# Kernel tuning notes

Hardware: AMD Instinct MI355X
Metric: run time of the kernel (lower is better)

The kernel has to match this reference:

```python
import jax, jax.numpy as jnp
import numpy as np
import math

L = 6          # num_layers
D = 512        # hidden_dim
S = 2048       # seq_len
B = 8          # batch
ODIM = 1       # output_dim
SCALES = (24.0, 720.0)


def setup_inputs() -> dict:
    key = jax.random.key(0)
    ks = jax.random.split(key, 12)
    def n(k, shape, scale=0.02):
        return jax.random.normal(k, shape, dtype=jnp.float32) * scale
    return {
        "z": jax.random.normal(ks[0], (B, S, 1), dtype=jnp.float32),
        "c": jax.random.normal(ks[1], (B, S, 1), dtype=jnp.float32),
        "enc_w": n(ks[2], (D, 2)), "enc_b": jnp.zeros((D,), jnp.float32),
        "beta": jnp.ones((L, len(SCALES)), jnp.float32),
        "wq": n(ks[3], (L, D, D)), "bq": jnp.zeros((L, D), jnp.float32),
        "wk": n(ks[4], (L, D, D)), "bk": jnp.zeros((L, D), jnp.float32),
        "wv": n(ks[5], (L, D, D)), "bv": jnp.zeros((L, D), jnp.float32),
        "ln1_w": jnp.ones((L, D), jnp.float32), "ln1_b": jnp.zeros((L, D), jnp.float32),
        "ln2_w": jnp.ones((L, D), jnp.float32), "ln2_b": jnp.zeros((L, D), jnp.float32),
        "ff1_w": n(ks[6], (L, 4 * D, D)), "ff1_b": jnp.zeros((L, 4 * D), jnp.float32),
        "ff2_w": n(ks[7], (L, D, 4 * D)), "ff2_b": jnp.zeros((L, D), jnp.float32),
        "out_w": n(ks[8], (ODIM, D)), "out_b": jnp.zeros((ODIM,), jnp.float32),
    }


def _ln(x, w, b, eps=1e-5):
    m = jnp.mean(x, axis=-1, keepdims=True)
    v = jnp.var(x, axis=-1, keepdims=True)
    return (x - m) * jax.lax.rsqrt(v + eps) * w + b


def _posenc(seq_len, dim):
    pos = jnp.arange(seq_len, dtype=jnp.float32)[:, None]
    div = jnp.exp(jnp.arange(0, dim, 2, dtype=jnp.float32) * (-(math.log(10000.0) / dim)))
    pe = jnp.zeros((seq_len, dim), jnp.float32)
    pe = pe.at[:, 0::2].set(jnp.sin(pos * div))
    pe = pe.at[:, 1::2].set(jnp.cos(pos * div))
    return pe


def reference(z, c, enc_w, enc_b, beta, wq, bq, wk, bk, wv, bv,
              ln1_w, ln1_b, ln2_w, ln2_b, ff1_w, ff1_b, ff2_w, ff2_b,
              out_w, out_b):
    # SequenceEncoder: cat(z,c) -> Linear(2, D) -> + sinusoidal PE
    x = jnp.concatenate([z, c], axis=-1) @ enc_w.T + enc_b       # [B,S,D]
    seq_len, d = x.shape[1], x.shape[2]
    x = x + _posenc(seq_len, d)[None]
    sqrt_d = math.sqrt(d)

    idx = jnp.arange(seq_len, dtype=jnp.float32)
    dist = jnp.abs(idx[:, None] - idx[None, :])                  # [S,S]

    for l in range(L):
        # pre-norm with ln1 (applied twice in the original code - replicated)
        xn = _ln(x, ln1_w[l], ln1_b[l])
        Q = xn @ wq[l].T + bq[l]
        K = xn @ wk[l].T + bk[l]
        V = xn @ wv[l].T + bv[l]
        attn = jnp.einsum('bid,bjd->bij', Q, K) / sqrt_d          # [B,S,S]
        bias = beta[l, 0] * jnp.cos(2.0 * math.pi * dist / SCALES[0]) \
             + beta[l, 1] * jnp.cos(2.0 * math.pi * dist / SCALES[1])
        probs = jax.nn.softmax(attn + bias, axis=-1)
        att_out = jnp.einsum('bij,bjd->bid', probs, V)
        # original applies layer_norm_1 again to the residual sum
        x = _ln(x + att_out, ln1_w[l], ln1_b[l])
        xn2 = _ln(x, ln2_w[l], ln2_b[l])
        h = jax.nn.relu(xn2 @ ff1_w[l].T + ff1_b[l])
        x = x + h @ ff2_w[l].T + ff2_b[l]

    return x @ out_w.T + out_b                                    # [B,S,ODIM]
```

## Files before the change

kernel.cpp:

```cpp
#include <hip/hip_runtime.h>
#include <math.h>

#define BB 8
#define SS 2048
#define DD 512
#define LL 6
#define FFD 2048

typedef _Float16 half_t;
typedef __attribute__((ext_vector_type(8))) _Float16 half8;
typedef __attribute__((ext_vector_type(4))) _Float16 half4;
typedef __attribute__((ext_vector_type(4))) float f32x4;

enum { EPI_NONE = 0, EPI_RELU = 2, EPI_RES = 3, EPI_ATTN = 4, EPI_QKV = 5, EPI_PV = 6 };

__device__ __forceinline__ void gl_lds16(const void* g, void* l) {
    __builtin_amdgcn_global_load_lds(
        (const __attribute__((address_space(1))) unsigned int*)g,
        (__attribute__((address_space(3))) unsigned int*)l,
        16, 0, 0);
}

__device__ __forceinline__ void blockReduce2(float& a, float& b, float* sm) {
#pragma unroll
    for (int off = 32; off; off >>= 1) {
        a += __shfl_down(a, off);
        b += __shfl_down(b, off);
    }
    int lane = threadIdx.x & 63;
    int w = threadIdx.x >> 6;
    if (lane == 0) { sm[w] = a; sm[4 + w] = b; }
    __syncthreads();
    a = sm[0] + sm[1] + sm[2] + sm[3];
    b = sm[4] + sm[5] + sm[6] + sm[7];
    __syncthreads();
}

__global__ __launch_bounds__(256) void encode_kernel(
    const float* __restrict__ z, const float* __restrict__ c,
    const float* __restrict__ enc_w, const float* __restrict__ enc_b,
    float* __restrict__ x)
{
    int idx = blockIdx.x * 256 + threadIdx.x;
    int d  = idx & (DD - 1);
    int bs = idx >> 9;
    int s  = bs & (SS - 1);
    float v = z[bs] * enc_w[2 * d] + c[bs] * enc_w[2 * d + 1] + enc_b[d];
    float div = expf(-(float)(d & ~1) * (9.210340371976184f / 512.0f));
    float ang = (float)s * div;
    v += (d & 1) ? cosf(ang) : sinf(ang);
    x[idx] = v;
}

__global__ __launch_bounds__(256) void convert_layer_kernel(
    const float* __restrict__ wq, const float* __restrict__ wk,
    const float* __restrict__ wv, const float* __restrict__ f1,
    const float* __restrict__ f2, half_t* __restrict__ wqkv,
    half_t* __restrict__ f1h, half_t* __restrict__ f2h)
{
    const int NQ = DD * DD;
    int i = blockIdx.x * 256 + threadIdx.x;
    if (i < 3 * NQ) {
        int which = i >> 18, j = i & (NQ - 1);
        const float* s = (which == 0) ? wq : (which == 1) ? wk : wv;
        wqkv[i] = (half_t)s[j];
    } else {
        int k = i - 3 * NQ;
        if (k < FFD * DD) f1h[k] = (half_t)f1[k];
        else              f2h[k - FFD * DD] = (half_t)f2[k - FFD * DD];
    }
}

__global__ __launch_bounds__(256) void bias_table_kernel(
    const float* __restrict__ beta, float* __restrict__ tbl)
{
    int i = blockIdx.x * 256 + threadIdx.x;
    int l = i >> 11, d = i & (SS - 1);
    tbl[i] = beta[2 * l] * cosf(0.2617993877991494f * d)
           + beta[2 * l + 1] * cosf(0.008726646259971648f * d);
}

__global__ __launch_bounds__(256) void ln_kernel(
    const float* __restrict__ src, const float* __restrict__ w,
    const float* __restrict__ b, half_t* __restrict__ dst)
{
    __shared__ float sm[8];
    size_t row = blockIdx.x;
    const float* p = src + row * DD;
    int t = threadIdx.x;
    float v0 = p[t], v1 = p[t + 256];
    float s = v0 + v1, sq = v0 * v0 + v1 * v1;
    blockReduce2(s, sq, sm);
    float mean = s * (1.0f / DD);
    float var  = sq * (1.0f / DD) - mean * mean;
    float rs   = rsqrtf(var + 1e-5f);
    dst[row * DD + t]       = (half_t)((v0 - mean) * rs * w[t] + b[t]);
    dst[row * DD + t + 256] = (half_t)((v1 - mean) * rs * w[t + 256] + b[t + 256]);
}

__global__ __launch_bounds__(256) void add_ln_ln_kernel(
    float* __restrict__ x, const half_t* __restrict__ att,
    const float* __restrict__ w1, const float* __restrict__ b1,
    const float* __restrict__ w2, const float* __restrict__ b2,
    half_t* __restrict__ xn)
{
    __shared__ float sm[8];
    size_t row = blockIdx.x;
    int t = threadIdx.x;
    float v0 = x[row * DD + t] + (float)att[row * DD + t];
    float v1 = x[row * DD + t + 256] + (float)att[row * DD + t + 256];
    float s = v0 + v1, sq = v0 * v0 + v1 * v1;
    blockReduce2(s, sq, sm);
    float mean = s * (1.0f / DD);
    float var  = sq * (1.0f / DD) - mean * mean;
    float rs   = rsqrtf(var + 1e-5f);
    float y0 = (v0 - mean) * rs * w1[t] + b1[t];
    float y1 = (v1 - mean) * rs * w1[t + 256] + b1[t + 256];
    x[row * DD + t]       = y0;
    x[row * DD + t + 256] = y1;
    s = y0 + y1; sq = y0 * y0 + y1 * y1;
    blockReduce2(s, sq, sm);
    mean = s * (1.0f / DD);
    var  = sq * (1.0f / DD) - mean * mean;
    rs   = rsqrtf(var + 1e-5f);
    xn[row * DD + t]       = (half_t)((y0 - mean) * rs * w2[t] + b2[t]);
    xn[row * DD + t + 256] = (half_t)((y1 - mean) * rs * w2[t + 256] + b2[t + 256]);
}

template<int MT, int EPI, bool OHALF, int SWZ = 0>
__global__ __launch_bounds__(256) void gemm_mfma(
    const half_t* __restrict__ A, const half_t* __restrict__ W,
    const float* __restrict__ bias, const float* __restrict__ res,
    void* __restrict__ Cp, int N, int K, float alpha,
    long long sA, long long sW, long long sC,
    const float* __restrict__ biasK, const float* __restrict__ biasV,
    half_t* __restrict__ Ck, half_t* __restrict__ Cv)
{
    constexpr int TM = MT / 32;
    constexpr int ABUF = MT * 32;
    constexpr int BBUF = 128 * 32;
    __shared__ __align__(16) half_t As[2 * ABUF];
    __shared__ __align__(16) half_t Bs[2 * BBUF];

    int bxi, byi, bzi;
    if (SWZ == 1) {
        const int id = blockIdx.x;
        const int cc = id & 7, rr = id >> 3;
        bxi = rr & 15;
        const int ss = cc + 8 * (rr >> 4);
        byi = ss & 15; bzi = ss >> 4;
    } else { bxi = blockIdx.x; byi = blockIdx.y; bzi = blockIdx.z; }

    const int z = bzi;
    A += (size_t)z * sA; W += (size_t)z * sW;
    float*  Cf = (float*)Cp  + (size_t)z * sC;
    half_t* Ch = (half_t*)Cp + (size_t)z * sC;

    const int tid = threadIdx.x;
    const int wv = tid >> 6, ln = tid & 63;
    const int bm = bxi * MT, bn = byi * 128;
    const int wm = (wv & 1) * (MT / 2), wn = (wv >> 1) * 64;

    const int srow = wv * 16 + (ln >> 2);
    const int scol = (ln & 3) * 8;
    const half_t* Ag = A + (size_t)(bm + srow) * K + scol;
    const half_t* Bg = W + (size_t)(bn + srow) * K + scol;

    f32x4 acc[TM][4] = {};
    float rs[TM];
#pragma unroll
    for (int i = 0; i < TM; ++i) rs[i] = 0.f;

    const int lane15 = ln & 15, quad = ln >> 4;
    const int koff = quad * 8;
    const int nIter = K >> 5;

    {
        char* a = (char*)As + wv * 1024;
        char* b = (char*)Bs + wv * 1024;
        gl_lds16(Ag, a);
        if (MT == 128) gl_lds16(Ag + (size_t)64 * K, a + 4096);
        gl_lds16(Bg, b);
        gl_lds16(Bg + (size_t)64 * K, b + 4096);
    }
    __syncthreads();

    for (int it = 0; it < nIter; ++it) {
        const int cur = it & 1;
        if (it + 1 < nIter) {
            const int k1 = (it + 1) << 5;
            char* a = (char*)As + (cur ^ 1) * (ABUF * 2) + wv * 1024;
            char* b = (char*)Bs + (cur ^ 1) * (BBUF * 2) + wv * 1024;
            gl_lds16(Ag + k1, a);
            if (MT == 128) gl_lds16(Ag + (size_t)64 * K + k1, a + 4096);
            gl_lds16(Bg + k1, b);
            gl_lds16(Bg + (size_t)64 * K + k1, b + 4096);
        }

        const half_t* Ab = As + cur * ABUF;
        const half_t* Bb = Bs + cur * BBUF;
        half8 aF[TM], bF[4];
#pragma unroll
        for (int i = 0; i < TM; ++i)
            aF[i] = *(const half8*)&Ab[(wm + i * 16 + lane15) * 32 + koff];
#pragma unroll
        for (int j = 0; j < 4; ++j)
            bF[j] = *(const half8*)&Bb[(wn + j * 16 + lane15) * 32 + koff];

        if (EPI == EPI_PV) {
#pragma unroll
            for (int i = 0; i < TM; ++i)
#pragma unroll
                for (int e = 0; e < 8; ++e) rs[i] += (float)aF[i][e];
        }

#pragma unroll
        for (int i = 0; i < TM; ++i)
#pragma unroll
            for (int j = 0; j < 4; ++j)
                acc[i][j] = __builtin_amdgcn_mfma_f32_16x16x32_f16(
                    aF[i], bF[j], acc[i][j], 0, 0, 0);

        __syncthreads();
    }

    float inv[TM][4];
    if (EPI == EPI_PV) {
#pragma unroll
        for (int i = 0; i < TM; ++i) {
            rs[i] += __shfl_xor(rs[i], 16);
            rs[i] += __shfl_xor(rs[i], 32);
            rs[i] = 1.0f / rs[i];
#pragma unroll
            for (int r = 0; r < 4; ++r)
                inv[i][r] = __shfl(rs[i], quad * 4 + r);
        }
    }

#pragma unroll
    for (int i = 0; i < TM; ++i) {
        const int m0 = bm + wm + i * 16 + quad * 4;
#pragma unroll
        for (int j = 0; j < 4; ++j) {
            const int gn = bn + wn + j * 16 + lane15;
            if (EPI == EPI_QKV) {
                const int seg = gn >> 9, nn = gn & (DD - 1);
                if (seg == 2) {
                    half4 pk;
#pragma unroll
                    for (int r = 0; r < 4; ++r)
                        pk[r] = (half_t)(acc[i][j][r] + biasV[nn]);
                    const int b = m0 >> 11, s0 = m0 & (SS - 1);
                    *(half4*)&Cv[((size_t)b * DD + nn) * SS + s0] = pk;
                } else {
                    const float bs = (seg == 0) ? bias[nn] : biasK[nn];
                    half_t* dst = (seg == 0) ? Ch : Ck;
#pragma unroll
                    for (int r = 0; r < 4; ++r)
                        dst[(size_t)(m0 + r) * DD + nn] = (half_t)(acc[i][j][r] + bs);
                }
            } else {
#pragma unroll
                for (int r = 0; r < 4; ++r) {
                    const int gm = m0 + r;
                    float v = acc[i][j][r];
                    if (EPI == EPI_ATTN) {
                        int dist = gm - gn; if (dist < 0) dist = -dist;
                        v = __expf(fminf(v * alpha + bias[dist], 10.0f));
                    } else if (EPI == EPI_PV) {
                        v *= inv[i][r];
                    } else {
                        if (EPI == EPI_RELU) v = fmaxf(v + bias[gn], 0.0f);
                        if (EPI == EPI_RES)  v += bias[gn] + res[(size_t)gm * N + gn];
                    }
                    if (OHALF) Ch[(size_t)gm * N + gn] = (half_t)v;
                    else       Cf[(size_t)gm * N + gn] = v;
                }
            }
        }
    }
}

__global__ __launch_bounds__(256) void out_kernel(
    const float* __restrict__ x, const float* __restrict__ ow,
    const float* __restrict__ ob, float* __restrict__ out)
{
    int row = blockIdx.x * 4 + (threadIdx.x >> 6);
    int lane = threadIdx.x & 63;
    const float* p = x + (size_t)row * DD;
    float s = 0.f;
#pragma unroll
    for (int k = 0; k < 8; ++k) s += p[lane + 64 * k] * ow[lane + 64 * k];
#pragma unroll
    for (int off = 32; off; off >>= 1) s += __shfl_down(s, off);
    if (lane == 0) out[row] = s + ob[0];
}

extern "C" void kernel_launch(void* const* d_in, const int* in_sizes, int n_in,
                              void* d_out, int out_size, void* d_ws, size_t ws_size,
                              hipStream_t stream)
{
    (void)in_sizes; (void)n_in; (void)out_size; (void)ws_size;
    const float* z     = (const float*)d_in[0];
    const float* c     = (const float*)d_in[1];
    const float* enc_w = (const float*)d_in[2];
    const float* enc_b = (const float*)d_in[3];
    const float* beta  = (const float*)d_in[4];
    const float* wq    = (const float*)d_in[5];
    const float* bq    = (const float*)d_in[6];
    const float* wk    = (const float*)d_in[7];
    const float* bk    = (const float*)d_in[8];
    const float* wv    = (const float*)d_in[9];
    const float* bv    = (const float*)d_in[10];
    const float* ln1w  = (const float*)d_in[11];
    const float* ln1b  = (const float*)d_in[12];
    const float* ln2w  = (const float*)d_in[13];
    const float* ln2b  = (const float*)d_in[14];
    const float* ff1w  = (const float*)d_in[15];
    const float* ff1b  = (const float*)d_in[16];
    const float* ff2w  = (const float*)d_in[17];
    const float* ff2b  = (const float*)d_in[18];
    const float* ow    = (const float*)d_in[19];
    const float* ob    = (const float*)d_in[20];

    const size_t BSD = (size_t)BB * SS * DD;
    const size_t BSS = (size_t)BB * SS * SS;

    char* p = (char*)d_ws;
    float*  x    = (float*)p;  p += BSD * 4;
    half_t* xnh  = (half_t*)p; p += BSD * 2;
    half_t* sch  = (half_t*)p; p += BSS * 2;
    char*   pool = p;          p += BSD * 2 * 4;
    half_t* atth = (half_t*)pool;
    half_t* qh   = (half_t*)(pool + BSD * 2);
    half_t* kh   = (half_t*)(pool + BSD * 4);
    half_t* vth  = (half_t*)(pool + BSD * 6);
    half_t* hh   = (half_t*)pool;
    half_t* wqkv = (half_t*)p; p += (size_t)3 * DD * DD * 2;
    half_t* f1h  = (half_t*)p; p += (size_t)FFD * DD * 2;
    half_t* f2h  = (half_t*)p; p += (size_t)FFD * DD * 2;
    float*  tbl  = (float*)p;

    const float alpha = 0.044194173824159216f;
    const int BS = BB * SS;
    const long long sQ = (long long)SS * DD, sP = (long long)SS * SS,
                    sV = (long long)DD * SS;
    const int CONV_BLKS = (3 * DD * DD + 2 * FFD * DD) / 256;

    bias_table_kernel<<<LL * SS / 256, 256, 0, stream>>>(beta, tbl);
    encode_kernel<<<BS * DD / 256, 256, 0, stream>>>(z, c, enc_w, enc_b, x);

    for (int l = 0; l < LL; ++l) {
        convert_layer_kernel<<<CONV_BLKS, 256, 0, stream>>>(
            wq + (size_t)l * DD * DD, wk + (size_t)l * DD * DD,
            wv + (size_t)l * DD * DD, ff1w + (size_t)l * FFD * DD,
            ff2w + (size_t)l * DD * FFD, wqkv, f1h, f2h);

        ln_kernel<<<BS, 256, 0, stream>>>(x, ln1w + l * DD, ln1b + l * DD, xnh);

        gemm_mfma<128, EPI_QKV, true><<<dim3(BS / 128, 12, 1), 256, 0, stream>>>(
            xnh, wqkv, bq + l * DD, nullptr, qh, DD, DD, 0, 0, 0, 0,
            bk + l * DD, bv + l * DD, kh, vth);

        gemm_mfma<128, EPI_ATTN, true, 1><<<dim3(2048, 1, 1), 256, 0, stream>>>(
            qh, kh, tbl + l * SS, nullptr, sch, SS, DD, alpha, sQ, sQ, sP,
            nullptr, nullptr, nullptr, nullptr);

        gemm_mfma<64, EPI_PV, true><<<dim3(SS / 64, DD / 128, BB), 256, 0, stream>>>(
            sch, vth, nullptr, nullptr, atth, DD, SS, 0, sP, sV, sQ,
            nullptr, nullptr, nullptr, nullptr);

        add_ln_ln_kernel<<<BS, 256, 0, stream>>>(x, atth, ln1w + l * DD, ln1b + l * DD,
                                                 ln2w + l * DD, ln2b + l * DD, xnh);

        gemm_mfma<128, EPI_RELU, true><<<dim3(BS / 128, FFD / 128, 1), 256, 0, stream>>>(
            xnh, f1h, ff1b + l * FFD, nullptr, hh, FFD, DD, 0, 0, 0, 0,
            nullptr, nullptr, nullptr, nullptr);
        gemm_mfma<64, EPI_RES, false><<<dim3(BS / 64, DD / 128, 1), 256, 0, stream>>>(
            hh, f2h, ff2b + l * DD, x, x, DD, FFD, 0, 0, 0, 0,
            nullptr, nullptr, nullptr, nullptr);
    }

    out_kernel<<<BS / 4, 256, 0, stream>>>(x, ow, ob, (float*)d_out);
}
```

Before: 1.976 ms.

## Run attention Q/K/V, scores and PV matmuls in FP8 e4m3 with fused residual

Result: slower. 2.018 ms (+2.2%).

```diff
diff --git a/kernel.cpp b/kernel.cpp
--- a/kernel.cpp
+++ b/kernel.cpp
@@ -1,4 +1,5 @@
 #include <hip/hip_runtime.h>
+#include <hip/hip_fp8.h>
 #include <math.h>
 
 #define BB 8
@@ -9,10 +10,18 @@
 
 typedef _Float16 half_t;
 typedef __attribute__((ext_vector_type(8))) _Float16 half8;
-typedef __attribute__((ext_vector_type(4))) _Float16 half4;
 typedef __attribute__((ext_vector_type(4))) float f32x4;
 
 enum { EPI_NONE = 0, EPI_RELU = 2, EPI_RES = 3, EPI_ATTN = 4, EPI_QKV = 5, EPI_PV = 6 };
+
+__device__ __forceinline__ unsigned char f2e4m3(float v) {
+    __hip_fp8_e4m3 f(v);
+    return f.__x;
+}
+__device__ __forceinline__ float e4m3_2f(unsigned char b) {
+    __hip_fp8_e4m3 f; f.__x = b;
+    return (float)f;
+}
 
 __device__ __forceinline__ void gl_lds16(const void* g, void* l) {
     __builtin_amdgcn_global_load_lds(
@@ -98,8 +107,8 @@
     dst[row * DD + t + 256] = (half_t)((v1 - mean) * rs * w[t + 256] + b[t + 256]);
 }
 
-__global__ __launch_bounds__(256) void add_ln_ln_kernel(
-    float* __restrict__ x, const half_t* __restrict__ att,
+__global__ __launch_bounds__(256) void ln_ln_kernel(
+    float* __restrict__ x,
     const float* __restrict__ w1, const float* __restrict__ b1,
     const float* __restrict__ w2, const float* __restrict__ b2,
     half_t* __restrict__ xn)
@@ -107,8 +116,8 @@
     __shared__ float sm[8];
     size_t row = blockIdx.x;
     int t = threadIdx.x;
-    float v0 = x[row * DD + t] + (float)att[row * DD + t];
-    float v1 = x[row * DD + t + 256] + (float)att[row * DD + t + 256];
+    float v0 = x[row * DD + t];
+    float v1 = x[row * DD + t + 256];
     float s = v0 + v1, sq = v0 * v0 + v1 * v1;
     blockReduce2(s, sq, sm);
     float mean = s * (1.0f / DD);
@@ -127,20 +136,21 @@
     xn[row * DD + t + 256] = (half_t)((y1 - mean) * rs * w2[t + 256] + b2[t + 256]);
 }
 
-template<int MT, int EPI, bool OHALF, int SWZ = 0>
+template<typename TIN, int MT, int EPI, int SWZ = 0>
 __global__ __launch_bounds__(256) void gemm_mfma(
-    const half_t* __restrict__ A, const half_t* __restrict__ W,
-    const float* __restrict__ bias, const float* __restrict__ res,
-    void* __restrict__ Cp, int N, int K, float alpha,
+    const void* __restrict__ Ap, const void* __restrict__ Wp,
+    const float* __restrict__ bias, void* __restrict__ Cp,
+    int N, int K, float alpha,
     long long sA, long long sW, long long sC,
     const float* __restrict__ biasK, const float* __restrict__ biasV,
-    half_t* __restrict__ Ck, half_t* __restrict__ Cv)
+    unsigned char* __restrict__ Ck, unsigned char* __restrict__ Cv)
 {
     constexpr int TM = MT / 32;
-    constexpr int ABUF = MT * 32;
-    constexpr int BBUF = 128 * 32;
-    __shared__ __align__(16) half_t As[2 * ABUF];
-    __shared__ __align__(16) half_t Bs[2 * BBUF];
+    constexpr int ES = (int)sizeof(TIN);
+    constexpr int ABYTES = MT * 32 * ES;
+    constexpr int BBYTES = 128 * 32 * ES;
+    __shared__ __align__(16) unsigned char As[2 * ABYTES];
+    __shared__ __align__(16) unsigned char Bs[2 * BBYTES];
 
     int bxi, byi, bzi;
     if (SWZ == 1) {
@@ -152,19 +162,21 @@
     } else { bxi = blockIdx.x; byi = blockIdx.y; bzi = blockIdx.z; }
 
     const int z = bzi;
-    A += (size_t)z * sA; W += (size_t)z * sW;
+    const unsigned char* A = (const unsigned char*)Ap + (size_t)z * sA * ES;
+    const unsigned char* W = (const unsigned char*)Wp + (size_t)z * sW * ES;
     float*  Cf = (float*)Cp  + (size_t)z * sC;
     half_t* Ch = (half_t*)Cp + (size_t)z * sC;
+    unsigned char* C8 = (unsigned char*)Cp + (size_t)z * sC;
 
     const int tid = threadIdx.x;
     const int wv = tid >> 6, ln = tid & 63;
     const int bm = bxi * MT, bn = byi * 128;
     const int wm = (wv & 1) * (MT / 2), wn = (wv >> 1) * 64;
 
-    const int srow = wv * 16 + (ln >> 2);
-    const int scol = (ln & 3) * 8;
-    const half_t* Ag = A + (size_t)(bm + srow) * K + scol;
-    const half_t* Bg = W + (size_t)(bn + srow) * K + scol;
+    const int srow  = (ES == 2) ? (wv * 16 + (ln >> 2)) : (wv * 32 + (ln >> 1));
+    const int scolB = (ES == 2) ? ((ln & 3) * 16) : ((ln & 1) * 16);
+    const unsigned char* Ag = A + (size_t)(bm + srow) * K * ES + scolB;
+    const unsigned char* Bg = W + (size_t)(bn + srow) * K * ES + scolB;
 
     f32x4 acc[TM][4] = {};
     float rs[TM];
@@ -172,54 +184,79 @@
     for (int i = 0; i < TM; ++i) rs[i] = 0.f;
 
     const int lane15 = ln & 15, quad = ln >> 4;
-    const int koff = quad * 8;
     const int nIter = K >> 5;
 
     {
-        char* a = (char*)As + wv * 1024;
-        char* b = (char*)Bs + wv * 1024;
-        gl_lds16(Ag, a);
-        if (MT == 128) gl_lds16(Ag + (size_t)64 * K, a + 4096);
-        gl_lds16(Bg, b);
-        gl_lds16(Bg + (size_t)64 * K, b + 4096);
+        unsigned char* la = As + wv * 1024;
+        unsigned char* lb = Bs + wv * 1024;
+        if (ES == 2) {
+            gl_lds16(Ag, la);
+            if (MT == 128) gl_lds16(Ag + (size_t)64 * K * ES, la + 4096);
+            gl_lds16(Bg, lb);
+            gl_lds16(Bg + (size_t)64 * K * ES, lb + 4096);
+        } else {
+            if (MT == 128 || wv < 2) gl_lds16(Ag, la);
+            gl_lds16(Bg, lb);
+        }
     }
     __syncthreads();
 
     for (int it = 0; it < nIter; ++it) {
         const int cur = it & 1;
         if (it + 1 < nIter) {
-            const int k1 = (it + 1) << 5;
-            char* a = (char*)As + (cur ^ 1) * (ABUF * 2) + wv * 1024;
-            char* b = (char*)Bs + (cur ^ 1) * (BBUF * 2) + wv * 1024;
-            gl_lds16(Ag + k1, a);
-            if (MT == 128) gl_lds16(Ag + (size_t)64 * K + k1, a + 4096);
-            gl_lds16(Bg + k1, b);
-            gl_lds16(Bg + (size_t)64 * K + k1, b + 4096);
-        }
-
-        const half_t* Ab = As + cur * ABUF;
-        const half_t* Bb = Bs + cur * BBUF;
+            const size_t ko = (size_t)(it + 1) * 32 * ES;
+            unsigned char* la = As + (cur ^ 1) * ABYTES + wv * 1024;
+            unsigned char* lb = Bs + (cur ^ 1) * BBYTES + wv * 1024;
+            if (ES == 2) {
+                gl_lds16(Ag + ko, la);
+                if (MT == 128) gl_lds16(Ag + (size_t)64 * K * ES + ko, la + 4096);
+                gl_lds16(Bg + ko, lb);
+                gl_lds16(Bg + (size_t)64 * K * ES + ko, lb + 4096);
+            } else {
+                if (MT == 128 || wv < 2) gl_lds16(Ag + ko, la);
+                gl_lds16(Bg + ko, lb);
+            }
+        }
+
+        const unsigned char* Ab = As + cur * ABYTES;
+        const unsigned char* Bb = Bs + cur * BBYTES;
         half8 aF[TM], bF[4];
+        long aF8[TM], bF8[4];
+#pragma unroll
+        for (int i = 0; i < TM; ++i) {
+            if constexpr (ES == 2)
+                aF[i] = *(const half8*)(Ab + ((wm + i * 16 + lane15) * 32 + quad * 8) * 2);
+            else
+                aF8[i] = *(const long*)(Ab + (wm + i * 16 + lane15) * 32 + quad * 8);
+        }
+#pragma unroll
+        for (int j = 0; j < 4; ++j) {
+            if constexpr (ES == 2)
+                bF[j] = *(const half8*)(Bb + ((wn + j * 16 + lane15) * 32 + quad * 8) * 2);
+            else
+                bF8[j] = *(const long*)(Bb + (wn + j * 16 + lane15) * 32 + quad * 8);
+        }
+
+        if (EPI == EPI_PV) {
+#pragma unroll
+            for (int i = 0; i < TM; ++i) {
+                union { long l; unsigned char b[8]; } u; u.l = aF8[i];
+#pragma unroll
+                for (int e = 0; e < 8; ++e) rs[i] += e4m3_2f(u.b[e]);
+            }
+        }
+
 #pragma unroll
         for (int i = 0; i < TM; ++i)
-            aF[i] = *(const half8*)&Ab[(wm + i * 16 + lane15) * 32 + koff];
-#pragma unroll
-        for (int j = 0; j < 4; ++j)
-            bF[j] = *(const half8*)&Bb[(wn + j * 16 + lane15) * 32 + koff];
-
-        if (EPI == EPI_PV) {
-#pragma unroll
-            for (int i = 0; i < TM; ++i)
-#pragma unroll
-                for (int e = 0; e < 8; ++e) rs[i] += (float)aF[i][e];
-        }
-
-#pragma unroll
-        for (int i = 0; i < TM; ++i)
-#pragma unroll
-            for (int j = 0; j < 4; ++j)
-                acc[i][j] = __builtin_amdgcn_mfma_f32_16x16x32_f16(
-                    aF[i], bF[j], acc[i][j], 0, 0, 0);
+#pragma unroll
+            for (int j = 0; j < 4; ++j) {
+                if constexpr (ES == 2)
+                    acc[i][j] = __builtin_amdgcn_mfma_f32_16x16x32_f16(
+                        aF[i], bF[j], acc[i][j], 0, 0, 0);
+                else
+                    acc[i][j] = __builtin_amdgcn_mfma_f32_16x16x32_fp8_fp8(
+                        aF8[i], bF8[j], acc[i][j], 0, 0, 0);
+            }
 
         __syncthreads();
     }
@@ -246,18 +283,18 @@
             if (EPI == EPI_QKV) {
                 const int seg = gn >> 9, nn = gn & (DD - 1);
                 if (seg == 2) {
-                    half4 pk;
+                    unsigned int pk = 0;
 #pragma unroll
                     for (int r = 0; r < 4; ++r)
-                        pk[r] = (half_t)(acc[i][j][r] + biasV[nn]);
+                        pk |= (unsigned int)f2e4m3(acc[i][j][r] + biasV[nn]) << (8 * r);
                     const int b = m0 >> 11, s0 = m0 & (SS - 1);
-                    *(half4*)&Cv[((size_t)b * DD + nn) * SS + s0] = pk;
+                    *(unsigned int*)&Cv[((size_t)b * DD + nn) * SS + s0] = pk;
                 } else {
                     const float bs = (seg == 0) ? bias[nn] : biasK[nn];
-                    half_t* dst = (seg == 0) ? Ch : Ck;
+                    unsigned char* dst = (seg == 0) ? C8 : Ck;
 #pragma unroll
                     for (int r = 0; r < 4; ++r)
-                        dst[(size_t)(m0 + r) * DD + nn] = (half_t)(acc[i][j][r] + bs);
+                        dst[(size_t)(m0 + r) * DD + nn] = f2e4m3(acc[i][j][r] + bs);
                 }
             } else {
 #pragma unroll
@@ -266,15 +303,17 @@
                     float v = acc[i][j][r];
                     if (EPI == EPI_ATTN) {
                         int dist = gm - gn; if (dist < 0) dist = -dist;
-                        v = __expf(fminf(v * alpha + bias[dist], 10.0f));
+                        v = __expf(fminf(v * alpha + bias[dist], 6.0f));
+                        C8[(size_t)gm * N + gn] = f2e4m3(v);
                     } else if (EPI == EPI_PV) {
-                        v *= inv[i][r];
+                        const size_t idx = (size_t)gm * N + gn;
+                        Cf[idx] = v * inv[i][r] + Cf[idx];
+                    } else if (EPI == EPI_RELU) {
+                        Ch[(size_t)gm * N + gn] = (half_t)fmaxf(v + bias[gn], 0.0f);
                     } else {
-                        if (EPI == EPI_RELU) v = fmaxf(v + bias[gn], 0.0f);
-                        if (EPI == EPI_RES)  v += bias[gn] + res[(size_t)gm * N + gn];
+                        const size_t idx = (size_t)gm * N + gn;
+                        Cf[idx] = v + bias[gn] + Cf[idx];
                     }
-                    if (OHALF) Ch[(size_t)gm * N + gn] = (half_t)v;
-                    else       Cf[(size_t)gm * N + gn] = v;
                 }
             }
         }
@@ -329,13 +368,11 @@
     char* p = (char*)d_ws;
     float*  x    = (float*)p;  p += BSD * 4;
     half_t* xnh  = (half_t*)p; p += BSD * 2;
-    half_t* sch  = (half_t*)p; p += BSS * 2;
-    char*   pool = p;          p += BSD * 2 * 4;
-    half_t* atth = (half_t*)pool;
-    half_t* qh   = (half_t*)(pool + BSD * 2);
-    half_t* kh   = (half_t*)(pool + BSD * 4);
-    half_t* vth  = (half_t*)(pool + BSD * 6);
-    half_t* hh   = (half_t*)pool;
+    unsigned char* sch = (unsigned char*)p; p += BSS;
+    unsigned char* qh  = (unsigned char*)p; p += BSD;
+    unsigned char* kh  = (unsigned char*)p; p += BSD;
+    unsigned char* vth = (unsigned char*)p; p += BSD;
+    half_t* hh   = (half_t*)p; p += (size_t)BB * SS * FFD * 2;
     half_t* wqkv = (half_t*)p; p += (size_t)3 * DD * DD * 2;
     half_t* f1h  = (half_t*)p; p += (size_t)FFD * DD * 2;
     half_t* f2h  = (half_t*)p; p += (size_t)FFD * DD * 2;
@@ -358,26 +395,26 @@
 
         ln_kernel<<<BS, 256, 0, stream>>>(x, ln1w + l * DD, ln1b + l * DD, xnh);
 
-        gemm_mfma<128, EPI_QKV, true><<<dim3(BS / 128, 12, 1), 256, 0, stream>>>(
-            xnh, wqkv, bq + l * DD, nullptr, qh, DD, DD, 0, 0, 0, 0,
+        gemm_mfma<half_t, 128, EPI_QKV><<<dim3(BS / 128, 12, 1), 256, 0, stream>>>(
+            xnh, wqkv, bq + l * DD, qh, 1536, DD, 0, 0, 0, 0,
             bk + l * DD, bv + l * DD, kh, vth);
 
-        gemm_mfma<128, EPI_ATTN, true, 1><<<dim3(2048, 1, 1), 256, 0, stream>>>(
-            qh, kh, tbl + l * SS, nullptr, sch, SS, DD, alpha, sQ, sQ, sP,
+        gemm_mfma<unsigned char, 128, EPI_ATTN, 1><<<dim3(2048, 1, 1), 256, 0, stream>>>(
+            qh, kh, tbl + l * SS, sch, SS, DD, alpha, sQ, sQ, sP,
             nullptr, nullptr, nullptr, nullptr);
 
-        gemm_mfma<64, EPI_PV, true><<<dim3(SS / 64, DD / 128, BB), 256, 0, stream>>>(
-            sch, vth, nullptr, nullptr, atth, DD, SS, 0, sP, sV, sQ,
+        gemm_mfma<unsigned char, 64, EPI_PV><<<dim3(SS / 64, DD / 128, BB), 256, 0, stream>>>(
+            sch, vth, nullptr, x, DD, SS, 0, sP, sV, sQ,
             nullptr, nullptr, nullptr, nullptr);
 
-        add_ln_ln_kernel<<<BS, 256, 0, stream>>>(x, atth, ln1w + l * DD, ln1b + l * DD,
-                                                 ln2w + l * DD, ln2b + l * DD, xnh);
-
-        gemm_mfma<128, EPI_RELU, true><<<dim3(BS / 128, FFD / 128, 1), 256, 0, stream>>>(
-            xnh, f1h, ff1b + l * FFD, nullptr, hh, FFD, DD, 0, 0, 0, 0,
+        ln_ln_kernel<<<BS, 256, 0, stream>>>(x, ln1w + l * DD, ln1b + l * DD,
+                                             ln2w + l * DD, ln2b + l * DD, xnh);
+
+        gemm_mfma<half_t, 128, EPI_RELU><<<dim3(BS / 128, FFD / 128, 1), 256, 0, stream>>>(
+            xnh, f1h, ff1b + l * FFD, hh, FFD, DD, 0, 0, 0, 0,
             nullptr, nullptr, nullptr, nullptr);
-        gemm_mfma<64, EPI_RES, false><<<dim3(BS / 64, DD / 128, 1), 256, 0, stream>>>(
-            hh, f2h, ff2b + l * DD, x, x, DD, FFD, 0, 0, 0, 0,
+        gemm_mfma<half_t, 64, EPI_RES><<<dim3(BS / 64, DD / 128, 1), 256, 0, stream>>>(
+            hh, f2h, ff2b + l * DD, x, DD, FFD, 0, 0, 0, 0,
             nullptr, nullptr, nullptr, nullptr);
     }
 
```
